# Kernel tuning notes

Hardware: AMD Instinct MI355X
Metric: run time of the kernel (lower is better)

Reference implementation:

```python
import jax, jax.numpy as jnp
import numpy as np

D_MODEL = 1024
N_HEADS = 16
HEAD_DIM = D_MODEL // N_HEADS


def apply_rope(x):
    # x: [B, S, H, Dh]; standard rotate-half RoPE over head_dim
    B, S, H, Dh = x.shape
    inv_freq = 1.0 / (10000.0 ** (jnp.arange(0, Dh, 2, dtype=jnp.float32) / Dh))  # [Dh/2]
    pos = jnp.arange(S, dtype=jnp.float32)
    freqs = pos[:, None] * inv_freq[None, :]          # [S, Dh/2]
    cos = jnp.cos(freqs)[None, :, None, :]            # [1, S, 1, Dh/2]
    sin = jnp.sin(freqs)[None, :, None, :]
    x1, x2 = x[..., :Dh // 2], x[..., Dh // 2:]
    return jnp.concatenate([x1 * cos - x2 * sin, x1 * sin + x2 * cos], axis=-1)


def setup_inputs() -> dict:
    key = jax.random.key(0)
    ks = jax.random.split(key, 8)
    B, S, D = 2, 2048, D_MODEL
    s = 0.02
    return {
        "query": jax.random.normal(ks[0], (B, S, D), dtype=jnp.float32),
        "key": jax.random.normal(ks[1], (B, S, D), dtype=jnp.float32),
        "value": jax.random.normal(ks[2], (B, S, D), dtype=jnp.float32),
        "Wq": jax.random.normal(ks[3], (D, D), dtype=jnp.float32) * s,
        "Wk": jax.random.normal(ks[4], (D, D), dtype=jnp.float32) * s,
        "Wv": jax.random.normal(ks[5], (D, D), dtype=jnp.float32) * s,
        "Wo": jax.random.normal(ks[6], (D, D), dtype=jnp.float32) * s,
        "bo": jax.random.normal(ks[7], (D,), dtype=jnp.float32) * s,
    }


def reference(query, key, value, Wq, Wk, Wv, Wo, bo):
    B, Sq, D = query.shape
    Skv = key.shape[1]
    H, Dh = N_HEADS, HEAD_DIM
    scale = Dh ** -0.5
    # projections (torch Linear: x @ W.T)
    q = (query @ Wq.T).reshape(B, Sq, H, Dh)
    k = (key @ Wk.T).reshape(B, Skv, H, Dh)
    v = (value @ Wv.T).reshape(B, Skv, H, Dh)
    q = apply_rope(q)
    k = apply_rope(k)
    # scores: [B, H, Sq, Skv]
    scores = jnp.einsum("bqhd,bkhd->bhqk", q, k) * scale
    attn_weights = jax.nn.softmax(scores, axis=-1)
    out = jnp.einsum("bhqk,bkhd->bqhd", attn_weights, v).reshape(B, Sq, D)
    out = out @ Wo.T + bo
    return out, attn_weights
```

## Files before the change

### kernel.cpp

```cpp
#include <hip/hip_runtime.h>
#include <math.h>

#define D_MODEL 1024
#define SEQ     2048
#define NB      2
#define NH      16
#define DH      64
#define ROWS    (NB*SEQ)
#define OUT_ELEMS ((size_t)ROWS*D_MODEL)

typedef short bf16x8 __attribute__((ext_vector_type(8)));
typedef short bf16x4 __attribute__((ext_vector_type(4)));
typedef float f32x4  __attribute__((ext_vector_type(4)));

#define AS1 __attribute__((address_space(1)))
#define AS3 __attribute__((address_space(3)))

__device__ __forceinline__ float bf2f(short u){
    union{float f; unsigned v;} x; x.v = ((unsigned)(unsigned short)u) << 16; return x.f;
}
__device__ __forceinline__ short f2bf(float f){
    union{float f; unsigned v;} x; x.f = f;
    unsigned r = (x.v + 0x7FFF + ((x.v >> 16) & 1)) >> 16;
    return (short)r;
}
__device__ __forceinline__ int swz8(int row, int slot){ return slot ^ ((row + (row>>3)) & 7); }

#define MFMA16(a,b,c) __builtin_amdgcn_mfma_f32_16x16x32_bf16((a),(b),(c),0,0,0)

__global__ __launch_bounds__(256) void conv_w(const float* __restrict__ Wq,
                                              const float* __restrict__ Wk,
                                              const float* __restrict__ Wv,
                                              const float* __restrict__ Wo,
                                              short* __restrict__ wqkv,
                                              short* __restrict__ wob)
{
    int i = blockIdx.x*256 + threadIdx.x;
    int sel = i >> 18;
    int loc = i & 262143;
    const float* src = sel==0 ? Wq : sel==1 ? Wk : sel==2 ? Wv : Wo;
    short* dst = sel < 3 ? wqkv + (size_t)sel*1048576 : wob;
    float4 v = *(const float4*)&src[(size_t)loc*4];
    bf16x4 o = { f2bf(v.x), f2bf(v.y), f2bf(v.z), f2bf(v.w) };
    *(bf16x4*)&dst[(size_t)loc*4] = o;
}

__global__ __launch_bounds__(256) void rope_table(float* __restrict__ tab)
{
    int i = blockIdx.x*256 + threadIdx.x;
    int j = i & 31, s = i >> 5;
    float ang = (float)s * exp2f(-(float)j * 0.41524101186092437f);
    float sn, cs; sincosf(ang, &sn, &cs);
    tab[(size_t)s*64 + j*2]     = cs;
    tab[(size_t)s*64 + j*2 + 1] = sn;
}

__global__ __launch_bounds__(256) void gemm_qkv(const float* __restrict__ qx,
                                                const float* __restrict__ kx,
                                                const float* __restrict__ vx,
                                                const short* __restrict__ wqkv,
                                                short* __restrict__ qkvb)
{
    const int z = blockIdx.z;
    const float* A = z==0 ? qx : z==1 ? kx : vx;
    const short* B = wqkv + (size_t)z*D_MODEL*D_MODEL;
    short*       C = qkvb + (size_t)z*OUT_ELEMS;

    __shared__ __align__(16) short Alds[128*32];
    __shared__ __align__(16) short Blds[128*32];
    const int t = threadIdx.x, lane = t & 63, wid = t >> 6;
    const int m0 = blockIdx.y << 7, n0 = blockIdx.x << 7;
    const int wm = (wid >> 1) << 6, wn = (wid & 1) << 6;
    const int l15 = lane & 15, l4 = lane >> 4;

    f32x4 acc[4][4] = {};

    for (int k0 = 0; k0 < D_MODEL; k0 += 32) {
        float4 ar[4];
        #pragma unroll
        for (int u = 0; u < 4; ++u) {
            int id = u*256 + t;
            int row = id >> 3, c4 = id & 7;
            ar[u] = *(const float4*)&A[(size_t)(m0+row)*D_MODEL + k0 + c4*4];
        }
        __syncthreads();
        #pragma unroll
        for (int u = 0; u < 4; ++u) {
            int id = u*256 + t;
            int row = id >> 3, c4 = id & 7;
            bf16x4 a4 = { f2bf(ar[u].x), f2bf(ar[u].y), f2bf(ar[u].z), f2bf(ar[u].w) };
            *(bf16x4*)&Alds[row*32 + c4*4] = a4;
        }
        #pragma unroll
        for (int u = 0; u < 2; ++u) {
            int row = (wid*2 + u)*16 + (lane >> 2);
            int kc  = k0 + (lane & 3)*8;
            const short* gb = &B[(size_t)(n0 + row)*D_MODEL + kc];
            __builtin_amdgcn_global_load_lds((const AS1 unsigned*)gb,
                (AS3 unsigned*)&Blds[(wid*2 + u)*512], 16, 0, 0);
        }
        __syncthreads();
        bf16x8 af[4], bfr[4];
        #pragma unroll
        for (int mf = 0; mf < 4; ++mf)
            af[mf] = *(const bf16x8*)&Alds[(wm + mf*16 + l15)*32 + l4*8];
        #pragma unroll
        for (int nf = 0; nf < 4; ++nf)
            bfr[nf] = *(const bf16x8*)&Blds[(wn + nf*16 + l15)*32 + l4*8];
        #pragma unroll
        for (int mf = 0; mf < 4; ++mf)
            #pragma unroll
            for (int nf = 0; nf < 4; ++nf)
                acc[mf][nf] = MFMA16(af[mf], bfr[nf], acc[mf][nf]);
    }

    #pragma unroll
    for (int nf = 0; nf < 4; ++nf) {
        int col = n0 + wn + nf*16 + l15;
        #pragma unroll
        for (int mf = 0; mf < 4; ++mf)
            #pragma unroll
            for (int j = 0; j < 4; ++j) {
                int row = m0 + wm + mf*16 + l4*4 + j;
                C[(size_t)row*D_MODEL + col] = f2bf(acc[mf][nf][j]);
            }
    }
}

__global__ __launch_bounds__(256) void gemm_out(const short* __restrict__ A,
                                                const short* __restrict__ B,
                                                const float* __restrict__ bias,
                                                float* __restrict__ Cout)
{
    __shared__ __align__(16) short Alds[128*32];
    __shared__ __align__(16) short Blds[128*32];
    const int t = threadIdx.x, lane = t & 63, wid = t >> 6;
    const int m0 = blockIdx.y << 7, n0 = blockIdx.x << 7;
    const int wm = (wid >> 1) << 6, wn = (wid & 1) << 6;
    const int l15 = lane & 15, l4 = lane >> 4;

    f32x4 acc[4][4] = {};

    for (int k0 = 0; k0 < D_MODEL; k0 += 32) {
        __syncthreads();
        #pragma unroll
        for (int u = 0; u < 2; ++u) {
            int row = (wid*2 + u)*16 + (lane >> 2);
            int kc  = k0 + (lane & 3)*8;
            const short* ga = &A[(size_t)(m0 + row)*D_MODEL + kc];
            const short* gb = &B[(size_t)(n0 + row)*D_MODEL + kc];
            __builtin_amdgcn_global_load_lds((const AS1 unsigned*)ga,
                (AS3 unsigned*)&Alds[(wid*2 + u)*512], 16, 0, 0);
            __builtin_amdgcn_global_load_lds((const AS1 unsigned*)gb,
                (AS3 unsigned*)&Blds[(wid*2 + u)*512], 16, 0, 0);
        }
        __syncthreads();
        bf16x8 af[4], bfr[4];
        #pragma unroll
        for (int mf = 0; mf < 4; ++mf)
            af[mf] = *(const bf16x8*)&Alds[(wm + mf*16 + l15)*32 + l4*8];
        #pragma unroll
        for (int nf = 0; nf < 4; ++nf)
            bfr[nf] = *(const bf16x8*)&Blds[(wn + nf*16 + l15)*32 + l4*8];
        #pragma unroll
        for (int mf = 0; mf < 4; ++mf)
            #pragma unroll
            for (int nf = 0; nf < 4; ++nf)
                acc[mf][nf] = MFMA16(af[mf], bfr[nf], acc[mf][nf]);
    }

    #pragma unroll
    for (int nf = 0; nf < 4; ++nf) {
        int col = n0 + wn + nf*16 + l15;
        float bv = bias[col];
        #pragma unroll
        for (int mf = 0; mf < 4; ++mf)
            #pragma unroll
            for (int j = 0; j < 4; ++j) {
                int row = m0 + wm + mf*16 + l4*4 + j;
                Cout[(size_t)row*D_MODEL + col] = acc[mf][nf][j] + bv;
            }
    }
}

__global__ __launch_bounds__(256) void rope_apply(short* __restrict__ q,
                                                  short* __restrict__ k,
                                                  const float* __restrict__ tab)
{
    int idx = blockIdx.x*256 + threadIdx.x;
    int c = idx & 3, h = (idx >> 2) & 15, bs = idx >> 6;
    int s = bs & (SEQ-1);
    size_t base = (size_t)bs*D_MODEL + h*DH + c*8;
    const float4* tp = (const float4*)&tab[(size_t)s*64 + c*16];
    float4 t0 = tp[0], t1 = tp[1], t2 = tp[2], t3 = tp[3];
    float cs[8] = {t0.x,t0.z,t1.x,t1.z,t2.x,t2.z,t3.x,t3.z};
    float sn[8] = {t0.y,t0.w,t1.y,t1.w,t2.y,t2.w,t3.y,t3.w};
    bf16x8 q1 = *(bf16x8*)&q[base], q2 = *(bf16x8*)&q[base+32];
    bf16x8 k1 = *(bf16x8*)&k[base], k2 = *(bf16x8*)&k[base+32];
    bf16x8 q1o, q2o, k1o, k2o;
    #pragma unroll
    for (int e = 0; e < 8; ++e) {
        float a = bf2f(q1[e]), b = bf2f(q2[e]);
        q1o[e] = f2bf(a*cs[e] - b*sn[e]); q2o[e] = f2bf(a*sn[e] + b*cs[e]);
        a = bf2f(k1[e]); b = bf2f(k2[e]);
        k1o[e] = f2bf(a*cs[e] - b*sn[e]); k2o[e] = f2bf(a*sn[e] + b*cs[e]);
    }
    *(bf16x8*)&q[base] = q1o; *(bf16x8*)&q[base+32] = q2o;
    *(bf16x8*)&k[base] = k1o; *(bf16x8*)&k[base+32] = k2o;
}

__global__ __launch_bounds__(512) void attn_fused(const short* __restrict__ qb,
                                                  const short* __restrict__ kb,
                                                  const short* __restrict__ vb,
                                                  float* __restrict__ attn,
                                                  short* __restrict__ aob)
{
    __shared__ __align__(16) short Klds[64*64];
    __shared__ __align__(16) short Vt  [64*64];
    __shared__ __align__(16) short Plds[8*16*64];
    const int t = threadIdx.x, lane = t & 63, wv = t >> 6;
    const int bid = blockIdx.x;
    const int nb = (bid & 7)*64 + (bid >> 3);
    const int rb = nb & 15, bh = nb >> 4;
    const int h = bh & 15;
    const size_t bs0 = (size_t)(bh >> 4) * SEQ;
    const int qrow0 = rb << 7;
    const int l15 = lane & 15, l4 = lane >> 4;
    const int srow = t >> 3, ssl = t & 7;

    bf16x8 qf[2];
    {
        int qrow = qrow0 + wv*16 + l15;
        const short* qp = &qb[(bs0 + qrow)*D_MODEL + h*DH + l4*8];
        qf[0] = *(const bf16x8*)&qp[0];
        qf[1] = *(const bf16x8*)&qp[32];
    }

    const short* kbase = &kb[(bs0 + srow)*D_MODEL + h*DH + ssl*8];
    const short* vbase = &vb[(bs0 + srow)*D_MODEL + h*DH + ssl*8];

    float m[4] = {-1e30f,-1e30f,-1e30f,-1e30f};
    float l[4] = {0.f, 0.f, 0.f, 0.f};

    bf16x8 kreg = *(const bf16x8*)&kbase[0];
    for (int kt = 0; kt < SEQ; kt += 64) {
        __syncthreads();
        *(bf16x8*)&Klds[srow*64 + swz8(srow, ssl)*8] = kreg;
        __syncthreads();
        if (kt + 64 < SEQ)
            kreg = *(const bf16x8*)&kbase[(size_t)(kt+64)*D_MODEL];
        f32x4 sc[4] = {};
        __builtin_amdgcn_s_setprio(1);
        #pragma unroll
        for (int kk = 0; kk < 2; ++kk)
            #pragma unroll
            for (int nf = 0; nf < 4; ++nf) {
                int krow = nf*16 + l15;
                bf16x8 kf = *(const bf16x8*)&Klds[krow*64 + swz8(krow, kk*4 + l4)*8];
                sc[nf] = MFMA16(qf[kk], kf, sc[nf]);
            }
        __builtin_amdgcn_s_setprio(0);
        #pragma unroll
        for (int j = 0; j < 4; ++j) {
            float v0 = sc[0][j]*0.125f, v1 = sc[1][j]*0.125f,
                  v2 = sc[2][j]*0.125f, v3 = sc[3][j]*0.125f;
            float mx = fmaxf(fmaxf(v0,v1), fmaxf(v2,v3));
            mx = fmaxf(mx, __shfl_xor(mx, 1));
            mx = fmaxf(mx, __shfl_xor(mx, 2));
            mx = fmaxf(mx, __shfl_xor(mx, 4));
            mx = fmaxf(mx, __shfl_xor(mx, 8));
            float mn = fmaxf(m[j], mx);
            float sm = __expf(v0-mn) + __expf(v1-mn) + __expf(v2-mn) + __expf(v3-mn);
            sm += __shfl_xor(sm, 1);
            sm += __shfl_xor(sm, 2);
            sm += __shfl_xor(sm, 4);
            sm += __shfl_xor(sm, 8);
            l[j] = l[j]*__expf(m[j]-mn) + sm;
            m[j] = mn;
        }
    }
    float li[4];
    #pragma unroll
    for (int j = 0; j < 4; ++j) li[j] = 1.0f / l[j];

    f32x4 o[4] = {};
    kreg = *(const bf16x8*)&kbase[0];
    bf16x8 vreg = *(const bf16x8*)&vbase[0];
    for (int kt = 0; kt < SEQ; kt += 64) {
        __syncthreads();
        *(bf16x8*)&Klds[srow*64 + swz8(srow, ssl)*8] = kreg;
        #pragma unroll
        for (int e = 0; e < 8; ++e) {
            int d = ssl*8 + e;
            Vt[d*64 + swz8(d, srow>>3)*8 + (srow&7)] = vreg[e];
        }
        __syncthreads();
        if (kt + 64 < SEQ) {
            kreg = *(const bf16x8*)&kbase[(size_t)(kt+64)*D_MODEL];
            vreg = *(const bf16x8*)&vbase[(size_t)(kt+64)*D_MODEL];
        }
        f32x4 sc[4] = {};
        __builtin_amdgcn_s_setprio(1);
        #pragma unroll
        for (int kk = 0; kk < 2; ++kk)
            #pragma unroll
            for (int nf = 0; nf < 4; ++nf) {
                int krow = nf*16 + l15;
                bf16x8 kf = *(const bf16x8*)&Klds[krow*64 + swz8(krow, kk*4 + l4)*8];
                sc[nf] = MFMA16(qf[kk], kf, sc[nf]);
            }
        __builtin_amdgcn_s_setprio(0);
        size_t rowbase = ((size_t)bh*SEQ + qrow0 + wv*16 + l4*4)*SEQ + kt + l15;
        #pragma unroll
        for (int nf = 0; nf < 4; ++nf) {
            #pragma unroll
            for (int j = 0; j < 4; ++j) {
                float w = __expf(sc[nf][j]*0.125f - m[j]) * li[j];
                __builtin_nontemporal_store(w, &attn[rowbase + (size_t)j*SEQ + nf*16]);
                int prow = l4*4 + j, pcol = nf*16 + l15;
                Plds[wv*1024 + prow*64 + swz8(prow, pcol>>3)*8 + (pcol&7)] = f2bf(w);
            }
        }
        __builtin_amdgcn_s_setprio(1);
        #pragma unroll
        for (int kk = 0; kk < 2; ++kk) {
            bf16x8 pa = *(const bf16x8*)&Plds[wv*1024 + l15*64 + swz8(l15, kk*4 + l4)*8];
            #pragma unroll
            for (int nf = 0; nf < 4; ++nf) {
                int d = nf*16 + l15;
                bf16x8 vf = *(const bf16x8*)&Vt[d*64 + swz8(d, kk*4 + l4)*8];
                o[nf] = MFMA16(pa, vf, o[nf]);
            }
        }
        __builtin_amdgcn_s_setprio(0);
    }
    #pragma unroll
    for (int nf = 0; nf < 4; ++nf)
        #pragma unroll
        for (int j = 0; j < 4; ++j) {
            int qr = qrow0 + wv*16 + l4*4 + j;
            aob[(bs0 + qr)*D_MODEL + h*DH + nf*16 + l15] = f2bf(o[nf][j]);
        }
}

extern "C" void kernel_launch(void* const* d_in, const int* in_sizes, int n_in,
                              void* d_out, int out_size, void* d_ws, size_t ws_size,
                              hipStream_t stream)
{
    const float* query = (const float*)d_in[0];
    const float* key_  = (const float*)d_in[1];
    const float* value = (const float*)d_in[2];
    const float* Wq    = (const float*)d_in[3];
    const float* Wk    = (const float*)d_in[4];
    const float* Wv    = (const float*)d_in[5];
    const float* Wo    = (const float*)d_in[6];
    const float* bo    = (const float*)d_in[7];

    float* out  = (float*)d_out;
    float* attn = out + OUT_ELEMS;

    short* wqkv = (short*)d_ws;
    short* wob  = wqkv + (size_t)3*1048576;
    short* qkvb = wob  + (size_t)1048576;
    short* qb   = qkvb;
    short* kb   = qb + OUT_ELEMS;
    short* vb   = kb + OUT_ELEMS;
    short* aob  = vb + OUT_ELEMS;
    float* tab  = (float*)(aob + OUT_ELEMS);

    dim3 blk(256);

    hipLaunchKernelGGL(conv_w, dim3(4096), blk, 0, stream, Wq, Wk, Wv, Wo, wqkv, wob);
    hipLaunchKernelGGL(rope_table, dim3(256), blk, 0, stream, tab);
    hipLaunchKernelGGL(gemm_qkv, dim3(8, 32, 3), blk, 0, stream,
                       query, key_, value, wqkv, qkvb);
    hipLaunchKernelGGL(rope_apply, dim3(1024), blk, 0, stream, qb, kb, tab);
    hipLaunchKernelGGL(attn_fused, dim3(512), dim3(512), 0, stream,
                       qb, kb, vb, attn, aob);
    hipLaunchKernelGGL(gemm_out, dim3(8, 32), blk, 0, stream, aob, wob, bo, out);
}
```

Measured before the change: 332.8 us.

## Fuse RoPE into QKV GEMM epilogue, store V transposed, transpose score MFMA

Applies RoPE inside the QKV GEMM epilogue, so the separate rope_apply kernel and its extra read-modify-write pass over Q and K go away. V is written head-major and transposed, letting the attention kernel fill its V tile with one vector LDS store instead of eight scalar ones. The score MFMA operands are swapped so each lane holds four consecutive keys of one query row; softmax stats become per-lane scalars and the attention weights go out as 16-byte nontemporal stores. The risk is the strided, uncoalesced scalar V-transpose stores in the GEMM epilogue.

```diff
diff --git a/kernel.cpp b/kernel.cpp
--- a/kernel.cpp
+++ b/kernel.cpp
@@ -59,12 +59,14 @@
                                                 const float* __restrict__ kx,
                                                 const float* __restrict__ vx,
                                                 const short* __restrict__ wqkv,
-                                                short* __restrict__ qkvb)
+                                                const float* __restrict__ tab,
+                                                short* __restrict__ qb,
+                                                short* __restrict__ kb,
+                                                short* __restrict__ vbt)
 {
     const int z = blockIdx.z;
     const float* A = z==0 ? qx : z==1 ? kx : vx;
     const short* B = wqkv + (size_t)z*D_MODEL*D_MODEL;
-    short*       C = qkvb + (size_t)z*OUT_ELEMS;
 
     __shared__ __align__(16) short Alds[128*32];
     __shared__ __align__(16) short Blds[128*32];
@@ -114,16 +116,38 @@
                 acc[mf][nf] = MFMA16(af[mf], bfr[nf], acc[mf][nf]);
     }
 
-    #pragma unroll
-    for (int nf = 0; nf < 4; ++nf) {
-        int col = n0 + wn + nf*16 + l15;
+    if (z < 2) {
+        short* C = z==0 ? qb : kb;
         #pragma unroll
         for (int mf = 0; mf < 4; ++mf)
             #pragma unroll
             for (int j = 0; j < 4; ++j) {
                 int row = m0 + wm + mf*16 + l4*4 + j;
-                C[(size_t)row*D_MODEL + col] = f2bf(acc[mf][nf][j]);
-            }
+                int s = row & (SEQ-1);
+                #pragma unroll
+                for (int p = 0; p < 2; ++p) {
+                    int d31 = p*16 + l15;
+                    float2 cs2 = *(const float2*)&tab[(size_t)s*64 + d31*2];
+                    float x1 = acc[mf][p][j], x2 = acc[mf][p+2][j];
+                    size_t rb = (size_t)row*D_MODEL + n0 + wn;
+                    C[rb + p*16 + l15]       = f2bf(x1*cs2.x - x2*cs2.y);
+                    C[rb + (p+2)*16 + l15]   = f2bf(x1*cs2.y + x2*cs2.x);
+                }
+            }
+    } else {
+        #pragma unroll
+        for (int nf = 0; nf < 4; ++nf) {
+            int col = n0 + wn + nf*16 + l15;
+            int hh = col >> 6, d = col & 63;
+            #pragma unroll
+            for (int mf = 0; mf < 4; ++mf)
+                #pragma unroll
+                for (int j = 0; j < 4; ++j) {
+                    int row = m0 + wm + mf*16 + l4*4 + j;
+                    int b = row >> 11, s = row & (SEQ-1);
+                    vbt[(((size_t)(b*NH + hh))*DH + d)*SEQ + s] = f2bf(acc[mf][nf][j]);
+                }
+        }
     }
 }
 
@@ -183,35 +207,9 @@
     }
 }
 
-__global__ __launch_bounds__(256) void rope_apply(short* __restrict__ q,
-                                                  short* __restrict__ k,
-                                                  const float* __restrict__ tab)
-{
-    int idx = blockIdx.x*256 + threadIdx.x;
-    int c = idx & 3, h = (idx >> 2) & 15, bs = idx >> 6;
-    int s = bs & (SEQ-1);
-    size_t base = (size_t)bs*D_MODEL + h*DH + c*8;
-    const float4* tp = (const float4*)&tab[(size_t)s*64 + c*16];
-    float4 t0 = tp[0], t1 = tp[1], t2 = tp[2], t3 = tp[3];
-    float cs[8] = {t0.x,t0.z,t1.x,t1.z,t2.x,t2.z,t3.x,t3.z};
-    float sn[8] = {t0.y,t0.w,t1.y,t1.w,t2.y,t2.w,t3.y,t3.w};
-    bf16x8 q1 = *(bf16x8*)&q[base], q2 = *(bf16x8*)&q[base+32];
-    bf16x8 k1 = *(bf16x8*)&k[base], k2 = *(bf16x8*)&k[base+32];
-    bf16x8 q1o, q2o, k1o, k2o;
-    #pragma unroll
-    for (int e = 0; e < 8; ++e) {
-        float a = bf2f(q1[e]), b = bf2f(q2[e]);
-        q1o[e] = f2bf(a*cs[e] - b*sn[e]); q2o[e] = f2bf(a*sn[e] + b*cs[e]);
-        a = bf2f(k1[e]); b = bf2f(k2[e]);
-        k1o[e] = f2bf(a*cs[e] - b*sn[e]); k2o[e] = f2bf(a*sn[e] + b*cs[e]);
-    }
-    *(bf16x8*)&q[base] = q1o; *(bf16x8*)&q[base+32] = q2o;
-    *(bf16x8*)&k[base] = k1o; *(bf16x8*)&k[base+32] = k2o;
-}
-
 __global__ __launch_bounds__(512) void attn_fused(const short* __restrict__ qb,
                                                   const short* __restrict__ kb,
-                                                  const short* __restrict__ vb,
+                                                  const short* __restrict__ vbt,
                                                   float* __restrict__ attn,
                                                   short* __restrict__ aob)
 {
@@ -236,11 +234,10 @@
         qf[1] = *(const bf16x8*)&qp[32];
     }
 
-    const short* kbase = &kb[(bs0 + srow)*D_MODEL + h*DH + ssl*8];
-    const short* vbase = &vb[(bs0 + srow)*D_MODEL + h*DH + ssl*8];
-
-    float m[4] = {-1e30f,-1e30f,-1e30f,-1e30f};
-    float l[4] = {0.f, 0.f, 0.f, 0.f};
+    const short* kbase  = &kb[(bs0 + srow)*D_MODEL + h*DH + ssl*8];
+    const short* vtbase = &vbt[((size_t)bh*DH + srow)*SEQ + ssl*8];
+
+    float m = -1e30f, l = 0.f;
 
     bf16x8 kreg = *(const bf16x8*)&kbase[0];
     for (int kt = 0; kt < SEQ; kt += 64) {
@@ -257,47 +254,43 @@
             for (int nf = 0; nf < 4; ++nf) {
                 int krow = nf*16 + l15;
                 bf16x8 kf = *(const bf16x8*)&Klds[krow*64 + swz8(krow, kk*4 + l4)*8];
-                sc[nf] = MFMA16(qf[kk], kf, sc[nf]);
+                sc[nf] = MFMA16(kf, qf[kk], sc[nf]);
             }
         __builtin_amdgcn_s_setprio(0);
-        #pragma unroll
-        for (int j = 0; j < 4; ++j) {
-            float v0 = sc[0][j]*0.125f, v1 = sc[1][j]*0.125f,
-                  v2 = sc[2][j]*0.125f, v3 = sc[3][j]*0.125f;
-            float mx = fmaxf(fmaxf(v0,v1), fmaxf(v2,v3));
-            mx = fmaxf(mx, __shfl_xor(mx, 1));
-            mx = fmaxf(mx, __shfl_xor(mx, 2));
-            mx = fmaxf(mx, __shfl_xor(mx, 4));
-            mx = fmaxf(mx, __shfl_xor(mx, 8));
-            float mn = fmaxf(m[j], mx);
-            float sm = __expf(v0-mn) + __expf(v1-mn) + __expf(v2-mn) + __expf(v3-mn);
-            sm += __shfl_xor(sm, 1);
-            sm += __shfl_xor(sm, 2);
-            sm += __shfl_xor(sm, 4);
-            sm += __shfl_xor(sm, 8);
-            l[j] = l[j]*__expf(m[j]-mn) + sm;
-            m[j] = mn;
-        }
-    }
-    float li[4];
-    #pragma unroll
-    for (int j = 0; j < 4; ++j) li[j] = 1.0f / l[j];
+        float tmax = -1e30f;
+        #pragma unroll
+        for (int nf = 0; nf < 4; ++nf)
+            #pragma unroll
+            for (int j = 0; j < 4; ++j)
+                tmax = fmaxf(tmax, sc[nf][j]*0.125f);
+        tmax = fmaxf(tmax, __shfl_xor(tmax, 16));
+        tmax = fmaxf(tmax, __shfl_xor(tmax, 32));
+        float mn = fmaxf(m, tmax);
+        float ts = 0.f;
+        #pragma unroll
+        for (int nf = 0; nf < 4; ++nf)
+            #pragma unroll
+            for (int j = 0; j < 4; ++j)
+                ts += __expf(sc[nf][j]*0.125f - mn);
+        ts += __shfl_xor(ts, 16);
+        ts += __shfl_xor(ts, 32);
+        l = l*__expf(m - mn) + ts;
+        m = mn;
+    }
+    const float li = 1.0f / l;
 
     f32x4 o[4] = {};
     kreg = *(const bf16x8*)&kbase[0];
-    bf16x8 vreg = *(const bf16x8*)&vbase[0];
+    bf16x8 vreg = *(const bf16x8*)&vtbase[0];
+    const size_t wrow = ((size_t)bh*SEQ + qrow0 + wv*16 + l15)*SEQ;
     for (int kt = 0; kt < SEQ; kt += 64) {
         __syncthreads();
         *(bf16x8*)&Klds[srow*64 + swz8(srow, ssl)*8] = kreg;
-        #pragma unroll
-        for (int e = 0; e < 8; ++e) {
-            int d = ssl*8 + e;
-            Vt[d*64 + swz8(d, srow>>3)*8 + (srow&7)] = vreg[e];
-        }
+        *(bf16x8*)&Vt  [srow*64 + swz8(srow, ssl)*8] = vreg;
         __syncthreads();
         if (kt + 64 < SEQ) {
             kreg = *(const bf16x8*)&kbase[(size_t)(kt+64)*D_MODEL];
-            vreg = *(const bf16x8*)&vbase[(size_t)(kt+64)*D_MODEL];
+            vreg = *(const bf16x8*)&vtbase[kt+64];
         }
         f32x4 sc[4] = {};
         __builtin_amdgcn_s_setprio(1);
@@ -307,18 +300,23 @@
             for (int nf = 0; nf < 4; ++nf) {
                 int krow = nf*16 + l15;
                 bf16x8 kf = *(const bf16x8*)&Klds[krow*64 + swz8(krow, kk*4 + l4)*8];
-                sc[nf] = MFMA16(qf[kk], kf, sc[nf]);
+                sc[nf] = MFMA16(kf, qf[kk], sc[nf]);
             }
         __builtin_amdgcn_s_setprio(0);
-        size_t rowbase = ((size_t)bh*SEQ + qrow0 + wv*16 + l4*4)*SEQ + kt + l15;
         #pragma unroll
         for (int nf = 0; nf < 4; ++nf) {
+            float w0 = __expf(sc[nf][0]*0.125f - m) * li;
+            float w1 = __expf(sc[nf][1]*0.125f - m) * li;
+            float w2 = __expf(sc[nf][2]*0.125f - m) * li;
+            float w3 = __expf(sc[nf][3]*0.125f - m) * li;
+            f32x4 wv4 = { w0, w1, w2, w3 };
+            __builtin_nontemporal_store(wv4,
+                (f32x4*)&attn[wrow + kt + nf*16 + l4*4]);
             #pragma unroll
             for (int j = 0; j < 4; ++j) {
-                float w = __expf(sc[nf][j]*0.125f - m[j]) * li[j];
-                __builtin_nontemporal_store(w, &attn[rowbase + (size_t)j*SEQ + nf*16]);
-                int prow = l4*4 + j, pcol = nf*16 + l15;
-                Plds[wv*1024 + prow*64 + swz8(prow, pcol>>3)*8 + (pcol&7)] = f2bf(w);
+                int k = nf*16 + l4*4 + j;
+                Plds[wv*1024 + l15*64 + swz8(l15, k>>3)*8 + (k&7)] =
+                    f2bf(j==0 ? w0 : j==1 ? w1 : j==2 ? w2 : w3);
             }
         }
         __builtin_amdgcn_s_setprio(1);
@@ -361,11 +359,10 @@
 
     short* wqkv = (short*)d_ws;
     short* wob  = wqkv + (size_t)3*1048576;
-    short* qkvb = wob  + (size_t)1048576;
-    short* qb   = qkvb;
+    short* qb   = wob  + (size_t)1048576;
     short* kb   = qb + OUT_ELEMS;
-    short* vb   = kb + OUT_ELEMS;
-    short* aob  = vb + OUT_ELEMS;
+    short* vbt  = kb + OUT_ELEMS;
+    short* aob  = vbt + OUT_ELEMS;
     float* tab  = (float*)(aob + OUT_ELEMS);
 
     dim3 blk(256);
@@ -373,9 +370,8 @@
     hipLaunchKernelGGL(conv_w, dim3(4096), blk, 0, stream, Wq, Wk, Wv, Wo, wqkv, wob);
     hipLaunchKernelGGL(rope_table, dim3(256), blk, 0, stream, tab);
     hipLaunchKernelGGL(gemm_qkv, dim3(8, 32, 3), blk, 0, stream,
-                       query, key_, value, wqkv, qkvb);
-    hipLaunchKernelGGL(rope_apply, dim3(1024), blk, 0, stream, qb, kb, tab);
+                       query, key_, value, wqkv, tab, qb, kb, vbt);
     hipLaunchKernelGGL(attn_fused, dim3(512), dim3(512), 0, stream,
-                       qb, kb, vb, attn, aob);
+                       qb, kb, vbt, attn, aob);
     hipLaunchKernelGGL(gemm_out, dim3(8, 32), blk, 0, stream, aob, wob, bo, out);
 }
```

Result: faster. 319.8 us (-3.9%).
